# Optimization experiments

Measured on AMD Instinct MI355X. Metric: run time of the kernel, lower is better.

The kernel has to match this reference:

```python
import jax, jax.numpy as jnp
import numpy as np

# Sparse MinkUNet-style backbone sizes
N0, N1, N2, N3 = 100000, 50000, 25000, 12500  # voxels per level (batch-concatenated)
K, KD = 27, 8        # 3x3x3 kernel offsets, stride-2 child offsets
B, S = 8, 1024       # batch, seed_num
C0, C1, C2, C3 = 32, 64, 128, 256
COUT = 512


def _w(k, shape, fan_in):
    return jax.random.normal(k, shape, dtype=jnp.float32) / np.sqrt(fan_in)


def setup_inputs() -> dict:
    key = jax.random.key(0)
    ks = jax.random.split(key, 32)
    inp = {}
    inp["feats"] = jax.random.normal(ks[0], (N0, 3), dtype=jnp.float32)
    # neighbor maps (kernel-offset gather indices, as built by a voxel hash map)
    inp["nbr0"] = jax.random.randint(ks[1], (N0, K), 0, N0, dtype=jnp.int32)
    inp["nbr1"] = jax.random.randint(ks[2], (N1, K), 0, N1, dtype=jnp.int32)
    inp["nbr2"] = jax.random.randint(ks[3], (N2, K), 0, N2, dtype=jnp.int32)
    inp["nbr3"] = jax.random.randint(ks[4], (N3, K), 0, N3, dtype=jnp.int32)
    # stride-2 downsample maps (coarse voxel -> fine children)
    inp["down1"] = jax.random.randint(ks[5], (N1, KD), 0, N0, dtype=jnp.int32)
    inp["down2"] = jax.random.randint(ks[6], (N2, KD), 0, N1, dtype=jnp.int32)
    inp["down3"] = jax.random.randint(ks[7], (N3, KD), 0, N2, dtype=jnp.int32)
    # nearest-parent upsample maps (fine voxel -> coarse parent)
    inp["up2"] = jax.random.randint(ks[8], (N2,), 0, N3, dtype=jnp.int32)
    inp["up1"] = jax.random.randint(ks[9], (N1,), 0, N2, dtype=jnp.int32)
    inp["up0"] = jax.random.randint(ks[10], (N0,), 0, N1, dtype=jnp.int32)
    # nearest-voxel devoxelize index for each FPS seed point
    inp["seed_idx"] = jax.random.randint(ks[11], (B, S), 0, N0, dtype=jnp.int32)
    # conv kernels [K, Cin, Cout] and 1x1 (linear) decoder weights
    inp["W_stem"] = _w(ks[12], (K, 3, C0), K * 3)
    inp["W_b0"] = _w(ks[13], (K, C0, C0), K * C0)
    inp["W_d1"] = _w(ks[14], (KD, C0, C1), KD * C0)
    inp["W_b1"] = _w(ks[15], (K, C1, C1), K * C1)
    inp["W_d2"] = _w(ks[16], (KD, C1, C2), KD * C1)
    inp["W_b2"] = _w(ks[17], (K, C2, C2), K * C2)
    inp["W_d3"] = _w(ks[18], (KD, C2, C3), KD * C2)
    inp["W_b3"] = _w(ks[19], (K, C3, C3), K * C3)
    inp["W_u2"] = _w(ks[20], (C3 + C2, 256), C3 + C2)
    inp["W_u1"] = _w(ks[21], (256 + C1, 128), 256 + C1)
    inp["W_u0"] = _w(ks[22], (128 + C0, 96), 128 + C0)
    inp["W_out"] = _w(ks[23], (96, COUT), 96)
    return inp


def sp_conv(f, nbr, W):
    # gather neighbor features then contract over (kernel offset, in-channel)
    g = f[nbr]                                # [N, K, Cin]
    return jnp.einsum('nkc,kco->no', g, W)    # [N, Cout]


def reference(feats, nbr0, nbr1, nbr2, nbr3, down1, down2, down3,
              up2, up1, up0, seed_idx,
              W_stem, W_b0, W_d1, W_b1, W_d2, W_b2, W_d3, W_b3,
              W_u2, W_u1, W_u0, W_out):
    relu = jax.nn.relu
    # encoder
    x0 = relu(sp_conv(feats, nbr0, W_stem))          # [N0, 32]
    x0 = x0 + relu(sp_conv(x0, nbr0, W_b0))
    x1 = relu(sp_conv(x0, down1, W_d1))              # [N1, 64]
    x1 = x1 + relu(sp_conv(x1, nbr1, W_b1))
    x2 = relu(sp_conv(x1, down2, W_d2))              # [N2, 128]
    x2 = x2 + relu(sp_conv(x2, nbr2, W_b2))
    x3 = relu(sp_conv(x2, down3, W_d3))              # [N3, 256]
    x3 = x3 + relu(sp_conv(x3, nbr3, W_b3))
    # decoder: nearest-parent upsample + skip concat + 1x1 conv
    u2 = relu(jnp.concatenate([x3[up2], x2], axis=-1) @ W_u2)   # [N2, 256]
    u1 = relu(jnp.concatenate([u2[up1], x1], axis=-1) @ W_u1)   # [N1, 128]
    u0 = relu(jnp.concatenate([u1[up0], x0], axis=-1) @ W_u0)   # [N0, 96]
    out_vox = u0 @ W_out                                        # [N0, 512]
    seed_feats = out_vox[seed_idx]                              # [B, S, 512]
    return jnp.transpose(seed_feats, (0, 2, 1))                 # [B, 512, S]
```

## Files before the change

### kernel.cpp

```cpp
#include <hip/hip_runtime.h>

typedef unsigned short u16;
typedef unsigned int u32;
typedef __bf16 bf16x8 __attribute__((ext_vector_type(8)));
typedef float f32x4 __attribute__((ext_vector_type(4)));
typedef u16 u16x4 __attribute__((ext_vector_type(4)));

#define NV0 100000
#define NV1 50000
#define NV2 25000
#define NV3 12500

enum : long {
  OFF_WB0  = 0,
  OFF_WD1  = 27648,
  OFF_WB1  = 44032,
  OFF_WD2  = 154624,
  OFF_WB2  = 220160,
  OFF_WD3  = 662528,
  OFF_WB3  = 924672,
  OFF_WU2  = 2694144,
  OFF_WU1  = 2792448,
  OFF_WU0  = 2833408,
  OFF_WOUT = 2848768,
  OFF_TA   = 2897920,
  OFF_X0   = OFF_TA  + 3200000,
  OFF_X1   = OFF_X0  + 3200000,
  OFF_X2   = OFF_X1  + 3200000,
  OFF_X3   = OFF_X2  + 3200000,
  OFF_U2   = OFF_X3  + 3200000,
  OFF_U1   = OFF_U2  + 6400000,
  OFF_U0S  = OFF_U1  + 6400000,
  OFF_END  = OFF_U0S + 786432,
};

__device__ __forceinline__ float b2f(u16 u) {
  union { u32 i; float f; } x; x.i = ((u32)u) << 16; return x.f;
}
__device__ __forceinline__ u16 f2b(float f) {
  union { float f; u32 i; } x; x.f = f;
  u32 r = (x.i + 0x7FFFu + ((x.i >> 16) & 1u)) >> 16;
  return (u16)r;
}
__device__ __forceinline__ void gload16(const u16* g, const u16* l) {
  __builtin_amdgcn_global_load_lds(
      (const __attribute__((address_space(1))) void*)g,
      (__attribute__((address_space(3))) void*)(u16*)l, 16, 0, 0);
}
__device__ __forceinline__ void store_out(u16* p, float v)  { *p = f2b(v); }
__device__ __forceinline__ void store_out(float* p, float v) { *p = v; }
constexpr int ilog2c(int x) { return x <= 1 ? 0 : 1 + ilog2c(x / 2); }

struct PD { const float* src; u16* dst; int KK, CIN, COUT; };
struct PrepArgs { PD d[11]; };

__global__ __launch_bounds__(256) void prep_k(PrepArgs pa) {
  const PD d = pa.d[blockIdx.y];
  const int cc = d.CIN * d.COUT;
  const int total = d.KK * cc;
  for (int e = blockIdx.x * 256 + threadIdx.x; e < total; e += gridDim.x * 256) {
    int k = e / cc;
    int r = e - k * cc;
    int c = r / d.COUT;
    int o = r - c * d.COUT;
    d.dst[(k * d.COUT + o) * d.CIN + c] = f2b(d.src[e]);
  }
}

__global__ __launch_bounds__(256) void stem_k(const float* __restrict__ feats,
                                              const int* __restrict__ nbr0,
                                              const float* __restrict__ wstem,
                                              u16* __restrict__ out) {
  __shared__ float Wl[27 * 3 * 32];
  const int tid = threadIdx.x;
  for (int i = tid; i < 2592; i += 256) Wl[i] = wstem[i];
  __syncthreads();
  const int n = blockIdx.x * 8 + (tid >> 5);
  const int o = tid & 31;
  if (n >= NV0) return;
  float acc = 0.f;
  const int* nb = nbr0 + n * 27;
  #pragma unroll
  for (int k = 0; k < 27; k++) {
    const int iv = nb[k];
    const float* f = feats + iv * 3;
    acc = fmaf(f[0], Wl[(k * 3 + 0) * 32 + o], acc);
    acc = fmaf(f[1], Wl[(k * 3 + 1) * 32 + o], acc);
    acc = fmaf(f[2], Wl[(k * 3 + 2) * 32 + o], acc);
  }
  out[n * 32 + o] = f2b(fmaxf(acc, 0.f));
}

template <int BM, int BN, int WM, int WN, int COUTF, int KCT, int BK, int MODE,
          int CIN, int KK, int CA, int KSPL, bool RES, bool DORELU, typename OT>
__global__ __launch_bounds__(256, 4) void gemm_k(
    const u16* __restrict__ src0, const u16* __restrict__ src1,
    const int* __restrict__ idx0, const int* __restrict__ idx1,
    const u16* __restrict__ wt, const u16* __restrict__ base,
    OT* __restrict__ out, int N) {
  constexpr int NWM = BM / WM, NWN = BN / WN;
  static_assert(NWM * NWN == 4, "4 waves");
  constexpr int MI = WM / 16, NI = WN / 16;
  constexpr int CB = KCT - CA;
  constexpr int SLOTS = BK / 8;
  constexpr int SM = SLOTS - 1;
  constexpr int LSL = ilog2c(SLOTS);
  constexpr int RPC = 64 / SLOTS;
  constexpr int LRPC = ilog2c(RPC);
  constexpr int ACH = (BM * BK) / 512;
  constexpr int BCH = (BN * BK) / 512;
  constexpr int NIT = KCT / BK / KSPL;
  constexpr int LOGC = ilog2c(CIN);
  constexpr int ATRIPS = ACH / 4;
  constexpr int CTRIPS = (ACH + BCH + 3) / 4;
  constexpr int NIDX = (MODE == 0) ? BM * KK : (MODE == 3 ? 1 : 2 * BM);
  static_assert(ACH % 4 == 0, "A chunks divisible by wave count");
  static_assert(KCT % (BK * KSPL) == 0, "K mult of BK*KSPL");
  static_assert((MODE != 1 && MODE != 2) || (CA % BK == 0), "concat boundary aligned");
  static_assert(KSPL == 1 || MODE == 0, "split only for sparse conv");

  __shared__ u16 As[2][BM * BK];
  __shared__ u16 Bs[2][BN * BK];
  __shared__ int Is[NIDX];
  const int tid = threadIdx.x;
  const int w = tid >> 6, lane = tid & 63;
  const int quad = lane >> 4, l16 = lane & 15;
  const int wm = w % NWM, wn = w / NWM;
  const int row0 = blockIdx.x * BM;
  const int col0 = blockIdx.y * BN;
  const int Nm1 = N - 1;
  const int srow = lane >> LSL;
  const int g    = (lane & SM) ^ (srow & SM);
  const int cl   = g * 8;

  if constexpr (MODE == 0) {
    for (int e = tid; e < BM * KK; e += 256) {
      const int r = e / KK, k = e - r * KK;
      int n = row0 + r; n = (n > Nm1) ? Nm1 : n;
      Is[e] = idx0[(long)n * KK + k] * CIN;
    }
  } else if constexpr (MODE == 1) {
    for (int e = tid; e < BM; e += 256) {
      int n = row0 + e; n = (n > Nm1) ? Nm1 : n;
      Is[e] = idx0[n] * CA;
      Is[BM + e] = n * CB;
    }
  } else if constexpr (MODE == 2) {
    for (int e = tid; e < BM; e += 256) {
      int n = row0 + e; n = (n > Nm1) ? Nm1 : n;
      const int s = idx0[n];
      Is[e] = idx1[s] * CA;
      Is[BM + e] = s * CB;
    }
  }
  if constexpr (MODE != 3) __syncthreads();

  int pre[CTRIPS];
  #pragma unroll
  for (int t = 0; t < CTRIPS; t++) {
    const int c = w + 4 * t;
    if (t < ATRIPS) {
      const int r = (c << LRPC) + srow;
      if constexpr (MODE == 0) {
        pre[t] = (r * KK + (cl >> LOGC)) * 4;
      } else if constexpr (MODE == 3) {
        int n = row0 + r; n = (n > Nm1) ? Nm1 : n;
        pre[t] = n * KCT + cl;
      } else {
        pre[t] = r * 4;
      }
    } else if (c < ACH + BCH) {
      const int o = col0 + ((c - ACH) << LRPC) + srow;
      if constexpr (MODE == 0)
        pre[t] = (cl >> LOGC) * (COUTF * CIN) + o * CIN + (cl & (CIN - 1));
      else
        pre[t] = o * KCT + cl;
    }
  }
  const int claneA = (MODE == 0) ? (cl & (CIN - 1)) : cl;

  f32x4 acc[MI][NI];
  #pragma unroll
  for (int i = 0; i < MI; i++)
    #pragma unroll
    for (int j = 0; j < NI; j++) acc[i][j] = {0.f, 0.f, 0.f, 0.f};

  auto stage = [&](int buf, int kc0) {
    int kadd = 0, cadd = 0, kcc = 0;
    const u16* sA = src0;
    if constexpr (MODE == 0) {
      kadd = (kc0 >> LOGC) * 4;
      cadd = kc0 & (CIN - 1);
      kcc  = (kc0 >> LOGC) * (COUTF * CIN) + cadd;
    } else if constexpr (MODE == 1 || MODE == 2) {
      if (kc0 >= CA) { kadd = BM * 4; cadd = kc0 - CA; sA = src1; }
      else           { cadd = kc0; }
    }
    #pragma unroll
    for (int t = 0; t < CTRIPS; t++) {
      const int c = w + 4 * t;
      if constexpr (CTRIPS * 4 > ACH + BCH) { if (c >= ACH + BCH) continue; }
      if (t < ATRIPS) {
        int off;
        if constexpr (MODE == 3) off = pre[t] + kc0;
        else off = *(const int*)((const char*)Is + (pre[t] + kadd)) + cadd + claneA;
        gload16(sA + off, &As[buf][c * 512]);
      } else {
        int off;
        if constexpr (MODE == 0) off = pre[t] + kcc;
        else                     off = pre[t] + kc0;
        gload16(wt + off, &Bs[buf][(c - ACH) * 512]);
      }
    }
  };

  const int kb = (KSPL > 1) ? (int)blockIdx.z * (KCT / KSPL) : 0;
  stage(0, kb);
  #pragma unroll 1
  for (int it = 0; it < NIT; it++) {
    __syncthreads();
    if (it + 1 < NIT) stage((it + 1) & 1, kb + (it + 1) * BK);
    const int buf = it & 1;
    #pragma unroll
    for (int kk = 0; kk < BK / 32; kk++) {
      bf16x8 af[MI], bfr[NI];
      #pragma unroll
      for (int i = 0; i < MI; i++) {
        const int row = wm * WM + i * 16 + l16;
        const int slot = row * SLOTS + (((kk << 2) + quad) ^ (row & SM));
        af[i] = *(const bf16x8*)&As[buf][slot * 8];
      }
      #pragma unroll
      for (int j = 0; j < NI; j++) {
        const int row = wn * WN + j * 16 + l16;
        const int slot = row * SLOTS + (((kk << 2) + quad) ^ (row & SM));
        bfr[j] = *(const bf16x8*)&Bs[buf][slot * 8];
      }
      #pragma unroll
      for (int i = 0; i < MI; i++)
        #pragma unroll
        for (int j = 0; j < NI; j++)
          acc[i][j] = __builtin_amdgcn_mfma_f32_16x16x32_bf16(af[i], bfr[j], acc[i][j], 0, 0, 0);
    }
  }

  OT* op = out;
  if constexpr (KSPL > 1) op += (long)blockIdx.z * ((long)N * COUTF);
  #pragma unroll
  for (int i = 0; i < MI; i++) {
    #pragma unroll
    for (int j = 0; j < NI; j++) {
      const int col = col0 + wn * WN + j * 16 + l16;
      #pragma unroll
      for (int r = 0; r < 4; r++) {
        const int n = row0 + wm * WM + i * 16 + quad * 4 + r;
        if (n < N) {
          float v = acc[i][j][r];
          if constexpr (RES)         v = b2f(base[(long)n * COUTF + col]) + fmaxf(v, 0.f);
          else if constexpr (DORELU) v = fmaxf(v, 0.f);
          store_out(&op[(long)n * COUTF + col], v);
        }
      }
    }
  }
}

__global__ __launch_bounds__(256) void fix_k(const float* __restrict__ p0,
                                             const float* __restrict__ p1,
                                             const u16* __restrict__ base,
                                             u16* __restrict__ out) {
  const long i = ((long)blockIdx.x * 256 + threadIdx.x) * 4;
  const f32x4 a = *(const f32x4*)(p0 + i);
  const f32x4 b = *(const f32x4*)(p1 + i);
  const u16x4 bs = *(const u16x4*)(base + i);
  u16x4 r;
  #pragma unroll
  for (int j = 0; j < 4; j++) r[j] = f2b(b2f(bs[j]) + fmaxf(a[j] + b[j], 0.f));
  *(u16x4*)(out + i) = r;
}

__global__ __launch_bounds__(256) void tout_k(const float* __restrict__ tmp,
                                              float* __restrict__ outp) {
  __shared__ float tl[64][65];
  const int tid = threadIdx.x;
  const int r0 = blockIdx.x * 64, o0 = blockIdx.y * 64;
  {
    const int rl = tid >> 2, oc = (tid & 3) * 16;
    const float* src = &tmp[(r0 + rl) * 512 + o0 + oc];
    #pragma unroll
    for (int j = 0; j < 16; j++) tl[rl][oc + j] = src[j];
  }
  __syncthreads();
  {
    const int ol = tid >> 2, sc = (tid & 3) * 16;
    const int b = r0 >> 10, s0 = r0 & 1023;
    float* dst = &outp[((long)b * 512 + (o0 + ol)) * 1024 + s0 + sc];
    #pragma unroll
    for (int j = 0; j < 16; j++) dst[j] = tl[sc + j][ol];
  }
}

extern "C" void kernel_launch(void* const* d_in, const int* in_sizes, int n_in,
                              void* d_out, int out_size, void* d_ws, size_t ws_size,
                              hipStream_t stream) {
  const float* feats = (const float*)d_in[0];
  const int* nbr0  = (const int*)d_in[1];
  const int* nbr1  = (const int*)d_in[2];
  const int* nbr2  = (const int*)d_in[3];
  const int* nbr3  = (const int*)d_in[4];
  const int* down1 = (const int*)d_in[5];
  const int* down2 = (const int*)d_in[6];
  const int* down3 = (const int*)d_in[7];
  const int* up2   = (const int*)d_in[8];
  const int* up1   = (const int*)d_in[9];
  const int* up0   = (const int*)d_in[10];
  const int* seed  = (const int*)d_in[11];
  u16* ws = (u16*)d_ws;

  PrepArgs pa;
  pa.d[0]  = {(const float*)d_in[13], ws + OFF_WB0,  27, 32, 32};
  pa.d[1]  = {(const float*)d_in[14], ws + OFF_WD1,  8,  32, 64};
  pa.d[2]  = {(const float*)d_in[15], ws + OFF_WB1,  27, 64, 64};
  pa.d[3]  = {(const float*)d_in[16], ws + OFF_WD2,  8,  64, 128};
  pa.d[4]  = {(const float*)d_in[17], ws + OFF_WB2,  27, 128, 128};
  pa.d[5]  = {(const float*)d_in[18], ws + OFF_WD3,  8,  128, 256};
  pa.d[6]  = {(const float*)d_in[19], ws + OFF_WB3,  27, 256, 256};
  pa.d[7]  = {(const float*)d_in[20], ws + OFF_WU2,  1,  384, 256};
  pa.d[8]  = {(const float*)d_in[21], ws + OFF_WU1,  1,  320, 128};
  pa.d[9]  = {(const float*)d_in[22], ws + OFF_WU0,  1,  160, 96};
  pa.d[10] = {(const float*)d_in[23], ws + OFF_WOUT, 1,  96,  512};
  prep_k<<<dim3(128, 11), 256, 0, stream>>>(pa);

  u16* ta  = ws + OFF_TA;
  u16* x0  = ws + OFF_X0;
  u16* x1  = ws + OFF_X1;
  u16* x2  = ws + OFF_X2;
  u16* x3  = ws + OFF_X3;
  u16* u2b = ws + OFF_U2;
  u16* u1b = ws + OFF_U1;
  u16* u0s = ws + OFF_U0S;
  float* tmp  = (float*)(ws + OFF_TA);
  float* part = (float*)(ws + OFF_U2);

  stem_k<<<12500, 256, 0, stream>>>(feats, nbr0, (const float*)d_in[12], ta);

  gemm_k<64, 32, 32, 16, 32, 864, 32, 0, 32, 27, 0, 1, true, true, u16>
      <<<dim3(1563, 1), 256, 0, stream>>>(ta, nullptr, nbr0, nullptr, ws + OFF_WB0, ta, x0, NV0);
  gemm_k<32, 64, 16, 32, 64, 256, 64, 0, 32, 8, 0, 1, false, true, u16>
      <<<dim3(1563, 1), 256, 0, stream>>>(x0, nullptr, down1, nullptr, ws + OFF_WD1, nullptr, ta, NV1);
  gemm_k<32, 64, 16, 32, 64, 1728, 64, 0, 64, 27, 0, 1, true, true, u16>
      <<<dim3(1563, 1), 256, 0, stream>>>(ta, nullptr, nbr1, nullptr, ws + OFF_WB1, ta, x1, NV1);
  gemm_k<32, 64, 16, 32, 128, 512, 64, 0, 64, 8, 0, 1, false, true, u16>
      <<<dim3(782, 2), 256, 0, stream>>>(x1, nullptr, down2, nullptr, ws + OFF_WD2, nullptr, ta, NV2);
  gemm_k<32, 64, 16, 32, 128, 3456, 64, 0, 128, 27, 0, 2, false, false, float>
      <<<dim3(782, 2, 2), 256, 0, stream>>>(ta, nullptr, nbr2, nullptr, ws + OFF_WB2, nullptr, part, NV2);
  fix_k<<<dim3(3125), 256, 0, stream>>>(part, part + 3200000, ta, x2);
  gemm_k<32, 64, 16, 32, 256, 1024, 64, 0, 128, 8, 0, 1, false, true, u16>
      <<<dim3(391, 4), 256, 0, stream>>>(x2, nullptr, down3, nullptr, ws + OFF_WD3, nullptr, ta, NV3);
  gemm_k<32, 64, 16, 32, 256, 6912, 64, 0, 256, 27, 0, 2, false, false, float>
      <<<dim3(391, 4, 2), 256, 0, stream>>>(ta, nullptr, nbr3, nullptr, ws + OFF_WB3, nullptr, part, NV3);
  fix_k<<<dim3(3125), 256, 0, stream>>>(part, part + 3200000, ta, x3);
  gemm_k<32, 64, 16, 32, 256, 384, 64, 1, 32, 1, 256, 1, false, true, u16>
      <<<dim3(782, 4), 256, 0, stream>>>(x3, x2, up2, nullptr, ws + OFF_WU2, nullptr, u2b, NV2);
  gemm_k<32, 64, 16, 32, 128, 320, 64, 1, 32, 1, 256, 1, false, true, u16>
      <<<dim3(1563, 2), 256, 0, stream>>>(u2b, x1, up1, nullptr, ws + OFF_WU1, nullptr, u1b, NV1);
  gemm_k<64, 96, 32, 48, 96, 160, 32, 2, 32, 1, 128, 1, false, true, u16>
      <<<dim3(128, 1), 256, 0, stream>>>(u1b, x0, seed, up0, ws + OFF_WU0, nullptr, u0s, 8192);
  gemm_k<64, 64, 32, 32, 512, 96, 32, 3, 32, 1, 0, 1, false, false, float>
      <<<dim3(128, 8), 256, 0, stream>>>(u0s, nullptr, nullptr, nullptr, ws + OFF_WOUT, nullptr, tmp, 8192);
  tout_k<<<dim3(128, 8), 256, 0, stream>>>(tmp, (float*)d_out);
}
```

Baseline: 556.3 us.

## Enlarge GEMM tiles and remap workgroups so column tiles share an XCD

The sparse-conv and decoder GEMMs move to larger tiles (64x64 with 32x32 per wave, 128x32 for the first block). This raises per-wave MFMA reuse and cuts the number of blocks that re-gather the same rows. A 1D swizzled grid maps blockIdx so that the column tiles and K-splits of a row tile land on the same XCD (wg&7 interleave), aiming to reuse gathered A rows in that XCD's L2. The larger tiles reduce parallelism on small levels and may increase register and LDS pressure.

New measurement: 490.8 us. 11.8% less time.

```diff
diff --git a/kernel.cpp b/kernel.cpp
--- a/kernel.cpp
+++ b/kernel.cpp
@@ -92,7 +92,8 @@
 }
 
 template <int BM, int BN, int WM, int WN, int COUTF, int KCT, int BK, int MODE,
-          int CIN, int KK, int CA, int KSPL, bool RES, bool DORELU, typename OT>
+          int CIN, int KK, int CA, int KSPL, int NCB, int SWZ,
+          bool RES, bool DORELU, typename OT>
 __global__ __launch_bounds__(256, 4) void gemm_k(
     const u16* __restrict__ src0, const u16* __restrict__ src1,
     const int* __restrict__ idx0, const int* __restrict__ idx1,
@@ -126,8 +127,24 @@
   const int w = tid >> 6, lane = tid & 63;
   const int quad = lane >> 4, l16 = lane & 15;
   const int wm = w % NWM, wn = w / NWM;
-  const int row0 = blockIdx.x * BM;
-  const int col0 = blockIdx.y * BN;
+
+  int row0, col0, kbz;
+  if constexpr (SWZ) {
+    const int NBR = (N + BM - 1) / BM;
+    const int R = NBR * KSPL;
+    const int wg = blockIdx.x;
+    const int xc = wg & 7, j = wg >> 3;
+    const int cb = j % NCB, t = j / NCB;
+    const int rt = t * 8 + xc;
+    if (rt >= R) return;
+    row0 = (rt / KSPL) * BM;
+    kbz  = rt % KSPL;
+    col0 = cb * BN;
+  } else {
+    row0 = blockIdx.x * BM;
+    col0 = blockIdx.y * BN;
+    kbz  = blockIdx.z;
+  }
   const int Nm1 = N - 1;
   const int srow = lane >> LSL;
   const int g    = (lane & SM) ^ (srow & SM);
@@ -214,7 +231,7 @@
     }
   };
 
-  const int kb = (KSPL > 1) ? (int)blockIdx.z * (KCT / KSPL) : 0;
+  const int kb = (KSPL > 1) ? kbz * (KCT / KSPL) : 0;
   stage(0, kb);
   #pragma unroll 1
   for (int it = 0; it < NIT; it++) {
@@ -245,7 +262,7 @@
   }
 
   OT* op = out;
-  if constexpr (KSPL > 1) op += (long)blockIdx.z * ((long)N * COUTF);
+  if constexpr (KSPL > 1) op += (long)kbz * ((long)N * COUTF);
   #pragma unroll
   for (int i = 0; i < MI; i++) {
     #pragma unroll
@@ -298,6 +315,12 @@
     #pragma unroll
     for (int j = 0; j < 16; j++) dst[j] = tl[sc + j][ol];
   }
+}
+
+static inline int swz_grid(int N, int BM, int KSPL, int NCB) {
+  const int nbr = (N + BM - 1) / BM;
+  const int rp = ((nbr * KSPL + 7) / 8) * 8;
+  return rp * NCB;
 }
 
 extern "C" void kernel_launch(void* const* d_in, const int* in_sizes, int n_in,
@@ -344,29 +367,29 @@
 
   stem_k<<<12500, 256, 0, stream>>>(feats, nbr0, (const float*)d_in[12], ta);
 
-  gemm_k<64, 32, 32, 16, 32, 864, 32, 0, 32, 27, 0, 1, true, true, u16>
-      <<<dim3(1563, 1), 256, 0, stream>>>(ta, nullptr, nbr0, nullptr, ws + OFF_WB0, ta, x0, NV0);
-  gemm_k<32, 64, 16, 32, 64, 256, 64, 0, 32, 8, 0, 1, false, true, u16>
-      <<<dim3(1563, 1), 256, 0, stream>>>(x0, nullptr, down1, nullptr, ws + OFF_WD1, nullptr, ta, NV1);
-  gemm_k<32, 64, 16, 32, 64, 1728, 64, 0, 64, 27, 0, 1, true, true, u16>
-      <<<dim3(1563, 1), 256, 0, stream>>>(ta, nullptr, nbr1, nullptr, ws + OFF_WB1, ta, x1, NV1);
-  gemm_k<32, 64, 16, 32, 128, 512, 64, 0, 64, 8, 0, 1, false, true, u16>
-      <<<dim3(782, 2), 256, 0, stream>>>(x1, nullptr, down2, nullptr, ws + OFF_WD2, nullptr, ta, NV2);
-  gemm_k<32, 64, 16, 32, 128, 3456, 64, 0, 128, 27, 0, 2, false, false, float>
-      <<<dim3(782, 2, 2), 256, 0, stream>>>(ta, nullptr, nbr2, nullptr, ws + OFF_WB2, nullptr, part, NV2);
+  gemm_k<128, 32, 32, 32, 32, 864, 32, 0, 32, 27, 0, 1, 1, 1, true, true, u16>
+      <<<swz_grid(NV0, 128, 1, 1), 256, 0, stream>>>(ta, nullptr, nbr0, nullptr, ws + OFF_WB0, ta, x0, NV0);
+  gemm_k<64, 64, 32, 32, 64, 256, 64, 0, 32, 8, 0, 1, 1, 1, false, true, u16>
+      <<<swz_grid(NV1, 64, 1, 1), 256, 0, stream>>>(x0, nullptr, down1, nullptr, ws + OFF_WD1, nullptr, ta, NV1);
+  gemm_k<64, 64, 32, 32, 64, 1728, 64, 0, 64, 27, 0, 1, 1, 1, true, true, u16>
+      <<<swz_grid(NV1, 64, 1, 1), 256, 0, stream>>>(ta, nullptr, nbr1, nullptr, ws + OFF_WB1, ta, x1, NV1);
+  gemm_k<64, 64, 32, 32, 128, 512, 64, 0, 64, 8, 0, 1, 2, 1, false, true, u16>
+      <<<swz_grid(NV2, 64, 1, 2), 256, 0, stream>>>(x1, nullptr, down2, nullptr, ws + OFF_WD2, nullptr, ta, NV2);
+  gemm_k<64, 64, 32, 32, 128, 3456, 64, 0, 128, 27, 0, 2, 2, 1, false, false, float>
+      <<<swz_grid(NV2, 64, 2, 2), 256, 0, stream>>>(ta, nullptr, nbr2, nullptr, ws + OFF_WB2, nullptr, part, NV2);
   fix_k<<<dim3(3125), 256, 0, stream>>>(part, part + 3200000, ta, x2);
-  gemm_k<32, 64, 16, 32, 256, 1024, 64, 0, 128, 8, 0, 1, false, true, u16>
-      <<<dim3(391, 4), 256, 0, stream>>>(x2, nullptr, down3, nullptr, ws + OFF_WD3, nullptr, ta, NV3);
-  gemm_k<32, 64, 16, 32, 256, 6912, 64, 0, 256, 27, 0, 2, false, false, float>
-      <<<dim3(391, 4, 2), 256, 0, stream>>>(ta, nullptr, nbr3, nullptr, ws + OFF_WB3, nullptr, part, NV3);
+  gemm_k<64, 64, 32, 32, 256, 1024, 64, 0, 128, 8, 0, 1, 4, 1, false, true, u16>
+      <<<swz_grid(NV3, 64, 1, 4), 256, 0, stream>>>(x2, nullptr, down3, nullptr, ws + OFF_WD3, nullptr, ta, NV3);
+  gemm_k<64, 64, 32, 32, 256, 6912, 64, 0, 256, 27, 0, 2, 4, 1, false, false, float>
+      <<<swz_grid(NV3, 64, 2, 4), 256, 0, stream>>>(ta, nullptr, nbr3, nullptr, ws + OFF_WB3, nullptr, part, NV3);
   fix_k<<<dim3(3125), 256, 0, stream>>>(part, part + 3200000, ta, x3);
-  gemm_k<32, 64, 16, 32, 256, 384, 64, 1, 32, 1, 256, 1, false, true, u16>
-      <<<dim3(782, 4), 256, 0, stream>>>(x3, x2, up2, nullptr, ws + OFF_WU2, nullptr, u2b, NV2);
-  gemm_k<32, 64, 16, 32, 128, 320, 64, 1, 32, 1, 256, 1, false, true, u16>
-      <<<dim3(1563, 2), 256, 0, stream>>>(u2b, x1, up1, nullptr, ws + OFF_WU1, nullptr, u1b, NV1);
-  gemm_k<64, 96, 32, 48, 96, 160, 32, 2, 32, 1, 128, 1, false, true, u16>
+  gemm_k<64, 64, 32, 32, 256, 384, 64, 1, 32, 1, 256, 1, 4, 1, false, true, u16>
+      <<<swz_grid(NV2, 64, 1, 4), 256, 0, stream>>>(x3, x2, up2, nullptr, ws + OFF_WU2, nullptr, u2b, NV2);
+  gemm_k<64, 64, 32, 32, 128, 320, 64, 1, 32, 1, 256, 1, 2, 1, false, true, u16>
+      <<<swz_grid(NV1, 64, 1, 2), 256, 0, stream>>>(u2b, x1, up1, nullptr, ws + OFF_WU1, nullptr, u1b, NV1);
+  gemm_k<64, 96, 32, 48, 96, 160, 32, 2, 32, 1, 128, 1, 1, 0, false, true, u16>
       <<<dim3(128, 1), 256, 0, stream>>>(u1b, x0, seed, up0, ws + OFF_WU0, nullptr, u0s, 8192);
-  gemm_k<64, 64, 32, 32, 512, 96, 32, 3, 32, 1, 0, 1, false, false, float>
+  gemm_k<64, 64, 32, 32, 512, 96, 32, 3, 32, 1, 0, 1, 1, 0, false, false, float>
       <<<dim3(128, 8), 256, 0, stream>>>(u0s, nullptr, nullptr, nullptr, ws + OFF_WOUT, nullptr, tmp, 8192);
   tout_k<<<dim3(128, 8), 256, 0, stream>>>(tmp, (float*)d_out);
 }
```
